# Kernel tuning notes

Hardware: AMD Instinct MI355X
Metric: run time of the kernel (lower is better)

## Reference

```python
import jax, jax.numpy as jnp
import numpy as np

B, N, D = 8, 1024, 768
H = 12
HD = D // H


def setup_inputs() -> dict:
    key = jax.random.key(0)
    ks = jax.random.split(key, 9)
    s = 1.0 / np.sqrt(D)
    return {
        "x": jax.random.normal(ks[0], (B, N, D), dtype=jnp.float32),
        "Wq": jax.random.normal(ks[1], (D, D), dtype=jnp.float32) * s,
        "bq": jax.random.normal(ks[2], (D,), dtype=jnp.float32) * 0.02,
        "Wk": jax.random.normal(ks[3], (D, D), dtype=jnp.float32) * s,
        "bk": jax.random.normal(ks[4], (D,), dtype=jnp.float32) * 0.02,
        "Wv": jax.random.normal(ks[5], (D, D), dtype=jnp.float32) * s,
        "bv": jax.random.normal(ks[6], (D,), dtype=jnp.float32) * 0.02,
        "Wo": jax.random.normal(ks[7], (D, D), dtype=jnp.float32) * s,
        "bo": jax.random.normal(ks[8], (D,), dtype=jnp.float32) * 0.02,
    }


def _softmax_one(x):
    # quiet softmax: exp(x - max) / (1 + sum exp(x - max))
    x = x - jnp.max(x, axis=-1, keepdims=True)
    ex = jnp.exp(x)
    return ex / (1.0 + jnp.sum(ex, axis=-1, keepdims=True))


def reference(x, Wq, bq, Wk, bk, Wv, bv, Wo, bo):
    q = x @ Wq + bq  # [B,N,D]
    k = x @ Wk + bk
    v = x @ Wv + bv
    # split heads -> [B,H,N,HD]
    qs = q.reshape(B, N, H, HD).transpose(0, 2, 1, 3)
    ks = k.reshape(B, N, H, HD).transpose(0, 2, 1, 3)
    vs = v.reshape(B, N, H, HD).transpose(0, 2, 1, 3)
    scores = jnp.einsum("bhqd,bhkd->bhqk", qs, ks) / np.sqrt(HD)
    attn = _softmax_one(scores)  # quiet_attention=True
    ctx = jnp.einsum("bhqk,bhkd->bhqd", attn, vs)
    ctx = ctx.transpose(0, 2, 1, 3).reshape(B, N, D)
    return ctx @ Wo + bo
```

## Files before the change

### kernel.cpp

```cpp
#include <hip/hip_runtime.h>
#include <cstdint>

#define DEV __device__ __forceinline__

typedef __bf16 bf16x4 __attribute__((ext_vector_type(4)));
typedef __bf16 bf16x8 __attribute__((ext_vector_type(8)));
typedef float  floatx4 __attribute__((ext_vector_type(4)));
typedef short  short4v __attribute__((ext_vector_type(4)));

constexpr int BB = 8, NSEQ = 1024, DMODEL = 768, NH = 12, HD = 64;
constexpr int MTOK = BB * NSEQ;
constexpr int NQKV = 3 * DMODEL;
constexpr float CS = 0.18033688011112042f;

DEV void async_copy16(void* lds, const void* g) {
    __builtin_amdgcn_global_load_lds(
        (__attribute__((address_space(1))) void*)(const_cast<void*>(g)),
        (__attribute__((address_space(3))) void*)lds,
        16, 0, 0);
}

DEV floatx4 mfma16x32(bf16x8 a, bf16x8 b, floatx4 c) {
    return __builtin_amdgcn_mfma_f32_16x16x32_bf16(a, b, c, 0, 0, 0);
}
DEV floatx4 mfma16x16(bf16x4 a, bf16x4 b, floatx4 c) {
    return __builtin_amdgcn_mfma_f32_16x16x16bf16_1k(
        __builtin_bit_cast(short4v, a), __builtin_bit_cast(short4v, b), c, 0, 0, 0);
}


__global__ __launch_bounds__(256) void k_prep(const float* __restrict__ x,
                                              __bf16* __restrict__ xb,
                                              const float* __restrict__ Wq,
                                              const float* __restrict__ Wk,
                                              const float* __restrict__ Wv,
                                              const float* __restrict__ Wo,
                                              __bf16* __restrict__ wtqkv,
                                              __bf16* __restrict__ wto,
                                              const float* __restrict__ bq,
                                              const float* __restrict__ bk,
                                              const float* __restrict__ bv,
                                              float* __restrict__ bqkv) {
    __shared__ float tile[32][33];
    int bid = blockIdx.x, t = threadIdx.x;
    if (bid < 6144) {
        int i = (bid * 256 + t) * 4;
        float4 v = *(const float4*)(x + i);
        bf16x4 o;
        o[0] = (__bf16)v.x; o[1] = (__bf16)v.y; o[2] = (__bf16)v.z; o[3] = (__bf16)v.w;
        *(bf16x4*)(xb + i) = o;
    } else if (bid < 8448) {
        int idx = bid - 6144;
        int z = idx / 576, rem = idx % 576;
        int k0 = (rem % 24) * 32, n0 = (rem / 24) * 32;
        const float* W = (z == 0) ? Wq : (z == 1) ? Wk : (z == 2) ? Wv : Wo;
        int tx = t & 31, ty = t >> 5;
#pragma unroll
        for (int p = 0; p < 4; p++)
            tile[ty + 8 * p][tx] = W[(size_t)(k0 + ty + 8 * p) * 768 + n0 + tx];
        __syncthreads();
        __bf16* out = (z < 3) ? (wtqkv + (size_t)z * 768 * 768) : wto;
#pragma unroll
        for (int p = 0; p < 4; p++)
            out[(size_t)(n0 + ty + 8 * p) * 768 + k0 + tx] = (__bf16)tile[tx][ty + 8 * p];
    } else {
        int i = (bid - 8448) * 256 + t;
        if (i < 768) bqkv[i] = bq[i];
        else if (i < 1536) bqkv[i] = bk[i - 768];
        else bqkv[i] = bv[i - 1536];
    }
}

__global__ __launch_bounds__(512) void k_qkv(const __bf16* __restrict__ A,
                                             const __bf16* __restrict__ Bt,
                                             const float* __restrict__ bias,
                                             __bf16* __restrict__ qfb,
                                             __bf16* __restrict__ kfb,
                                             __bf16* __restrict__ vfb) {
    constexpr int SLOT = 24576;
    __shared__ __align__(16) __bf16 lds[3 * SLOT];
    int t = threadIdx.x, lane = t & 63, w = t >> 6;
    int quad = lane >> 4, n16 = lane & 15;
    int wm = w >> 1, wn = w & 1;
    int m0 = blockIdx.x * 256, n0 = blockIdx.y * 128;
    floatx4 acc[4][4] = {};

    auto stage_part = [&](__bf16* slot, int k0, int p) {
        __bf16* As_ = slot;
        __bf16* Bs_ = slot + 16384;
#pragma unroll
        for (int i = 2 * p; i < 2 * p + 2; i++) {
            int off = t + i * 512;
            int row = off >> 3, pc = off & 7;
            int c = pc ^ (row & 7);
            async_copy16(&As_[row * 64 + pc * 8],
                         &A[(size_t)(m0 + row) * 768 + k0 + c * 8]);
        }
        {
            int off = t + p * 512;
            int row = off >> 3, pc = off & 7;
            int c = pc ^ (row & 7);
            async_copy16(&Bs_[row * 64 + pc * 8],
                         &Bt[(size_t)(n0 + row) * 768 + k0 + c * 8]);
        }
    };

    stage_part(lds, 0, 0);
    stage_part(lds, 0, 1);
    stage_part(lds + SLOT, 64, 0);
    stage_part(lds + SLOT, 64, 1);
    asm volatile("s_waitcnt vmcnt(6)\n\ts_barrier" ::: "memory");
    __builtin_amdgcn_sched_barrier(0);

#pragma unroll
    for (int kt = 0; kt < 12; kt++) {
        __bf16* As_ = lds + (kt % 3) * SLOT;
        __bf16* Bs_ = As_ + 16384;
        __bf16* pf = lds + ((kt + 2) % 3) * SLOT;
        int pk0 = (kt + 2) * 64;
        bool do_pf = (kt + 2 < 12);

#pragma unroll
        for (int kfi = 0; kfi < 2; kfi++) {
            if (do_pf) stage_part(pf, pk0, kfi);
            bf16x8 a[4], bfr[4];
#pragma unroll
            for (int rt = 0; rt < 4; rt++) {
                int row = wm * 64 + rt * 16 + n16;
                a[rt] = *(const bf16x8*)&As_[row * 64 + ((quad + 4 * kfi) ^ (row & 7)) * 8];
            }
#pragma unroll
            for (int ct = 0; ct < 4; ct++) {
                int row = wn * 64 + ct * 16 + n16;
                bfr[ct] = *(const bf16x8*)&Bs_[row * 64 + ((quad + 4 * kfi) ^ (row & 7)) * 8];
            }
            __builtin_amdgcn_s_setprio(1);
#pragma unroll
            for (int rt = 0; rt < 4; rt++)
#pragma unroll
                for (int ct = 0; ct < 4; ct++)
                    acc[rt][ct] = mfma16x32(a[rt], bfr[ct], acc[rt][ct]);
            __builtin_amdgcn_s_setprio(0);
        }

        if (kt < 11) {
            __builtin_amdgcn_sched_barrier(0);
            if (kt < 10) {
                asm volatile("s_waitcnt vmcnt(6)\n\ts_barrier" ::: "memory");
            } else {
                asm volatile("s_waitcnt vmcnt(0)\n\ts_barrier" ::: "memory");
            }
            __builtin_amdgcn_sched_barrier(0);
        }
    }

    if (n0 >= 1536) {
#pragma unroll
        for (int ct = 0; ct < 4; ct++) {
            int col = n0 + wn * 64 + ct * 16 + n16;
            float bs = bias[col];
            int cz = col - 1536;
            int hh = cz >> 6, hd = cz & 63;
            int mg = hd >> 4, l16 = hd & 15;
#pragma unroll
            for (int rt = 0; rt < 4; rt++) {
                int row0 = m0 + wm * 64 + rt * 16 + quad * 4;
                int bb = row0 >> 10, key = row0 & 1023;
                int ktv = key >> 6, wv = (key >> 4) & 3, qd = (key >> 2) & 3;
                bf16x4 pk;
#pragma unroll
                for (int r = 0; r < 4; r++) pk[r] = (__bf16)(acc[rt][ct][r] + bs);
                size_t idx = ((((size_t)(bb * 12 + hh) * 16 + ktv) * 4 + wv) * 4 + mg) * 256
                             + (size_t)(qd * 16 + l16) * 4;
                *(bf16x4*)&vfb[idx] = pk;
            }
        }
    } else {
        __bf16* dst = (n0 < 768) ? qfb : kfb;
        float mult = (n0 < 768) ? CS : 1.0f;
        int cofs = (n0 < 768) ? 0 : 768;
#pragma unroll
        for (int ct = 0; ct < 4; ct++) {
            int col = n0 + wn * 64 + ct * 16 + n16;
            float bs = bias[col];
            int cz = col - cofs;
            int hh = cz >> 6, hd = cz & 63;
            int kfi = hd >> 5, qd2 = (hd >> 3) & 3, j = hd & 7;
#pragma unroll
            for (int rt = 0; rt < 4; rt++) {
                int row0 = m0 + wm * 64 + rt * 16 + quad * 4;
                int bb = row0 >> 10, q = row0 & 1023;
                int t16 = q >> 4, nn = q & 15;
                size_t idx = (((size_t)(bb * 12 + hh) * 64 + t16) * 2 + kfi) * 512
                             + (size_t)(qd2 * 16 + nn) * 8 + j;
#pragma unroll
                for (int r = 0; r < 4; r++)
                    dst[idx + (size_t)r * 8] = (__bf16)((acc[rt][ct][r] + bs) * mult);
            }
        }
    }
}

template <typename OutT, bool QKV, int BN>
__global__ __launch_bounds__(256) void k_gemm(const __bf16* __restrict__ A,
                                              const __bf16* __restrict__ Bt,
                                              const float* __restrict__ bias,
                                              OutT* __restrict__ C, int Nn,
                                              __bf16* __restrict__ qfb,
                                              __bf16* __restrict__ kfb,
                                              __bf16* __restrict__ vfb) {
    constexpr int CT = BN / 32;
    constexpr int NBI = BN / 32;
    __shared__ __align__(16) __bf16 As[128 * 64];
    __shared__ __align__(16) __bf16 Bs[BN * 64];
    int t = threadIdx.x, lane = t & 63, w = t >> 6;
    int quad = lane >> 4, n16 = lane & 15;
    int wm = w & 1, wn = w >> 1;
    int m0 = blockIdx.x * 128, n0 = blockIdx.y * BN;
    floatx4 acc[4][CT] = {};

    for (int k0 = 0; k0 < 768; k0 += 64) {
        __syncthreads();
#pragma unroll
        for (int i = 0; i < 4; i++) {
            int off = t + i * 256;
            int row = off >> 3, pc = off & 7;
            int c = pc ^ (row & 7);
            async_copy16(&As[row * 64 + pc * 8],
                         &A[(size_t)(m0 + row) * 768 + k0 + c * 8]);
        }
#pragma unroll
        for (int i = 0; i < NBI; i++) {
            int off = t + i * 256;
            int row = off >> 3, pc = off & 7;
            int c = pc ^ (row & 7);
            async_copy16(&Bs[row * 64 + pc * 8],
                         &Bt[(size_t)(n0 + row) * 768 + k0 + c * 8]);
        }
        __builtin_amdgcn_s_waitcnt(0);
        __syncthreads();
#pragma unroll
        for (int kfi = 0; kfi < 2; kfi++) {
            bf16x8 a[4], bfr[CT];
#pragma unroll
            for (int rt = 0; rt < 4; rt++) {
                int row = wm * 64 + rt * 16 + n16;
                a[rt] = *(const bf16x8*)&As[row * 64 + ((quad + 4 * kfi) ^ (row & 7)) * 8];
            }
#pragma unroll
            for (int ct = 0; ct < CT; ct++) {
                int row = wn * (BN / 2) + ct * 16 + n16;
                bfr[ct] = *(const bf16x8*)&Bs[row * 64 + ((quad + 4 * kfi) ^ (row & 7)) * 8];
            }
#pragma unroll
            for (int rt = 0; rt < 4; rt++)
#pragma unroll
                for (int ct = 0; ct < CT; ct++)
                    acc[rt][ct] = mfma16x32(a[rt], bfr[ct], acc[rt][ct]);
        }
    }

    if (QKV) {
    } else {
#pragma unroll
        for (int ct = 0; ct < CT; ct++) {
            int col = n0 + wn * (BN / 2) + ct * 16 + n16;
            float bs = bias[col];
#pragma unroll
            for (int rt = 0; rt < 4; rt++) {
#pragma unroll
                for (int r = 0; r < 4; r++) {
                    int row = m0 + wm * 64 + rt * 16 + quad * 4 + r;
                    C[(size_t)row * Nn + col] = (OutT)(acc[rt][ct][r] + bs);
                }
            }
        }
    }
}

__global__ __launch_bounds__(256) void k_attn(const __bf16* __restrict__ QF,
                                              const __bf16* __restrict__ KF,
                                              const __bf16* __restrict__ VF,
                                              __bf16* __restrict__ ctx) {
    __shared__ __align__(16) unsigned char smem[18432];
    float* buf0 = (float*)smem;
    float* buf1 = (float*)(smem + 8704);
    float* Lsum = (float*)(smem + 17408);
    float* Pmax = (float*)(smem + 17920);

    int t = threadIdx.x, lane = t & 63, w = t >> 6;
    int quad = lane >> 4, n16 = lane & 15;
    int id = blockIdx.x;
    int bB = id & 7;
    int seq = id >> 3;
    int h = seq % 12;
    int qt = seq / 12;
    int q0 = qt * 32;
    int bh = bB * NH + h;

    bf16x8 qf[2][2];
    {
        const __bf16* qp = QF + (size_t)(bh * 64 + qt * 2) * 1024 + lane * 8;
#pragma unroll
        for (int ng = 0; ng < 2; ng++)
#pragma unroll
            for (int kfi = 0; kfi < 2; kfi++)
                qf[ng][kfi] = *(const bf16x8*)(qp + (ng * 2 + kfi) * 512);
    }
    const __bf16* kp = KF + (size_t)(bh * 64 + w) * 1024 + lane * 8;
    const __bf16* vp = VF + ((size_t)bh * 16 * 4 + w) * 1024 + lane * 4;

    floatx4 acc[4][2] = {};
    float rs[2] = {0.f, 0.f};
    float pm[2] = {0.f, 0.f};

    auto compute = [&](bf16x8 (&kf)[2], bf16x4 (&vf)[4]) {
        floatx4 s[2] = {};
#pragma unroll
        for (int ng = 0; ng < 2; ng++)
#pragma unroll
            for (int kfi = 0; kfi < 2; kfi++)
                s[ng] = mfma16x32(kf[kfi], qf[ng][kfi], s[ng]);
        bf16x4 pb[2];
#pragma unroll
        for (int ng = 0; ng < 2; ng++) {
#pragma unroll
            for (int r = 0; r < 4; r++) {
                float p = __builtin_amdgcn_exp2f(s[ng][r]);
                rs[ng] += p;
                pm[ng] = fmaxf(pm[ng], p);
                pb[ng][r] = (__bf16)p;
            }
        }
#pragma unroll
        for (int mg = 0; mg < 4; mg++)
#pragma unroll
            for (int ng = 0; ng < 2; ng++)
                acc[mg][ng] = mfma16x16(vf[mg], pb[ng], acc[mg][ng]);
    };

    bf16x8 kf0[2], kf1[2];
    bf16x4 vf0[4], vf1[4];
    kf0[0] = *(const bf16x8*)kp;
    kf0[1] = *(const bf16x8*)(kp + 512);
#pragma unroll
    for (int mg = 0; mg < 4; mg++) vf0[mg] = *(const bf16x4*)(vp + mg * 256);
    kp += 4096; vp += 4096;

    for (int kt = 0; kt < 16; kt += 2) {
        kf1[0] = *(const bf16x8*)kp;
        kf1[1] = *(const bf16x8*)(kp + 512);
#pragma unroll
        for (int mg = 0; mg < 4; mg++) vf1[mg] = *(const bf16x4*)(vp + mg * 256);
        kp += 4096; vp += 4096;
        compute(kf0, vf0);
        if (kt < 14) {
            kf0[0] = *(const bf16x8*)kp;
            kf0[1] = *(const bf16x8*)(kp + 512);
#pragma unroll
            for (int mg = 0; mg < 4; mg++) vf0[mg] = *(const bf16x4*)(vp + mg * 256);
            kp += 4096; vp += 4096;
        }
        compute(kf1, vf1);
    }

#pragma unroll
    for (int ng = 0; ng < 2; ng++) {
        rs[ng] += __shfl_xor(rs[ng], 16);
        rs[ng] += __shfl_xor(rs[ng], 32);
        pm[ng] = fmaxf(pm[ng], __shfl_xor(pm[ng], 16));
        pm[ng] = fmaxf(pm[ng], __shfl_xor(pm[ng], 32));
    }
    if (quad < 2) {
        Lsum[w * 32 + quad * 16 + n16] = quad ? rs[1] : rs[0];
        Pmax[w * 32 + quad * 16 + n16] = quad ? pm[1] : pm[0];
    }
    __syncthreads();

    float* mybuf = (w & 1) ? buf1 : buf0;
    if (w < 2) {
#pragma unroll
        for (int mg = 0; mg < 4; mg++)
#pragma unroll
            for (int ng = 0; ng < 2; ng++)
                *(floatx4*)&mybuf[(ng * 16 + n16) * 68 + mg * 16 + quad * 4] = acc[mg][ng];
    }
    __syncthreads();
    if (w >= 2) {
#pragma unroll
        for (int mg = 0; mg < 4; mg++)
#pragma unroll
            for (int ng = 0; ng < 2; ng++) {
                float* p = &mybuf[(ng * 16 + n16) * 68 + mg * 16 + quad * 4];
                floatx4 cur = *(const floatx4*)p;
                *(floatx4*)p = cur + acc[mg][ng];
            }
    }
    __syncthreads();

    int qrow = t >> 3;
    int hh = (t & 7) * 8;
    float l = Lsum[qrow] + Lsum[32 + qrow] + Lsum[64 + qrow] + Lsum[96 + qrow];
    float pmx = fmaxf(fmaxf(Pmax[qrow], Pmax[32 + qrow]),
                      fmaxf(Pmax[64 + qrow], Pmax[96 + qrow]));
    float invd = 1.f / (pmx + l);
    floatx4 v0 = *(const floatx4*)&buf0[qrow * 68 + hh];
    floatx4 v1 = *(const floatx4*)&buf0[qrow * 68 + hh + 4];
    floatx4 u0 = *(const floatx4*)&buf1[qrow * 68 + hh];
    floatx4 u1 = *(const floatx4*)&buf1[qrow * 68 + hh + 4];
    bf16x8 o;
#pragma unroll
    for (int j = 0; j < 4; j++) o[j] = (__bf16)((v0[j] + u0[j]) * invd);
#pragma unroll
    for (int j = 0; j < 4; j++) o[j + 4] = (__bf16)((v1[j] + u1[j]) * invd);
    __bf16* dst = ctx + (size_t)(bB * NSEQ + q0 + qrow) * DMODEL + h * 64 + hh;
    *(bf16x8*)dst = o;
}

extern "C" void kernel_launch(void* const* d_in, const int* in_sizes, int n_in,
                              void* d_out, int out_size, void* d_ws, size_t ws_size,
                              hipStream_t stream) {
    (void)in_sizes; (void)n_in; (void)out_size;
    const float* x  = (const float*)d_in[0];
    const float* Wq = (const float*)d_in[1];
    const float* bq = (const float*)d_in[2];
    const float* Wk = (const float*)d_in[3];
    const float* bk = (const float*)d_in[4];
    const float* Wv = (const float*)d_in[5];
    const float* bv = (const float*)d_in[6];
    const float* Wo = (const float*)d_in[7];
    const float* bo = (const float*)d_in[8];
    float* out = (float*)d_out;

    char* ws = (char*)d_ws;
    size_t off = 0;
    auto alloc = [&](size_t bytes) {
        void* p = ws + off;
        off += (bytes + 255) & ~(size_t)255;
        return p;
    };
    __bf16* xb    = (__bf16*)alloc((size_t)MTOK * DMODEL * 2);
    __bf16* wtqkv = (__bf16*)alloc((size_t)NQKV * DMODEL * 2);
    __bf16* wto   = (__bf16*)alloc((size_t)DMODEL * DMODEL * 2);
    float*  bqkv  = (float*)alloc((size_t)NQKV * 4);
    __bf16* qfb   = (__bf16*)alloc((size_t)MTOK * DMODEL * 2);
    __bf16* kfb   = (__bf16*)alloc((size_t)MTOK * DMODEL * 2);
    __bf16* vfb   = (__bf16*)alloc((size_t)MTOK * DMODEL * 2);
    if (off > ws_size) return;
    __bf16* ctx = xb;

    k_prep<<<dim3(8457), dim3(256), 0, stream>>>(x, xb, Wq, Wk, Wv, Wo, wtqkv, wto,
                                                 bq, bk, bv, bqkv);
    k_qkv<<<dim3(32, 18), dim3(512), 0, stream>>>(xb, wtqkv, bqkv, qfb, kfb, vfb);
    k_attn<<<dim3(3072), dim3(256), 0, stream>>>(qfb, kfb, vfb, ctx);
    k_gemm<float, false, 64><<<dim3(64, 12), dim3(256), 0, stream>>>(
        ctx, wto, bo, out, DMODEL, nullptr, nullptr, nullptr);
}
```

Measured before the change: 205.9 us.

## Switch attention to 32x32x16 MFMA with register-resident P via permlane swap

Rewrites the attention inner loop to use 32x32x16 bf16 MFMA instead of 16x16 tiles. The softmax probabilities are packed with v_cvt_pk_bf16_f32 and rearranged with v_permlane32_swap so P can feed the PV MFMA directly from registers. The Q/K/V store layouts in the QKV GEMM epilogue are changed to match the new fragment shapes. The aim is fewer MFMA issues and fewer per-element operations in the loop. It drops the sync before writing Lsum/Pmax, which relies on a later barrier for correctness.

```diff
diff --git a/kernel.cpp b/kernel.cpp
--- a/kernel.cpp
+++ b/kernel.cpp
@@ -6,7 +6,8 @@
 typedef __bf16 bf16x4 __attribute__((ext_vector_type(4)));
 typedef __bf16 bf16x8 __attribute__((ext_vector_type(8)));
 typedef float  floatx4 __attribute__((ext_vector_type(4)));
-typedef short  short4v __attribute__((ext_vector_type(4)));
+typedef float  floatx16 __attribute__((ext_vector_type(16)));
+typedef unsigned uint4v __attribute__((ext_vector_type(4)));
 
 constexpr int BB = 8, NSEQ = 1024, DMODEL = 768, NH = 12, HD = 64;
 constexpr int MTOK = BB * NSEQ;
@@ -23,9 +24,16 @@
 DEV floatx4 mfma16x32(bf16x8 a, bf16x8 b, floatx4 c) {
     return __builtin_amdgcn_mfma_f32_16x16x32_bf16(a, b, c, 0, 0, 0);
 }
-DEV floatx4 mfma16x16(bf16x4 a, bf16x4 b, floatx4 c) {
-    return __builtin_amdgcn_mfma_f32_16x16x16bf16_1k(
-        __builtin_bit_cast(short4v, a), __builtin_bit_cast(short4v, b), c, 0, 0, 0);
+DEV floatx16 mfma32x16(bf16x8 a, bf16x8 b, floatx16 c) {
+    return __builtin_amdgcn_mfma_f32_32x32x16_bf16(a, b, c, 0, 0, 0);
+}
+DEV unsigned cvtpk(float a, float b) {
+    unsigned r;
+    asm("v_cvt_pk_bf16_f32 %0, %1, %2" : "=v"(r) : "v"(a), "v"(b));
+    return r;
+}
+DEV void swap32(unsigned& x, unsigned& y) {
+    asm("v_permlane32_swap_b32 %0, %1" : "+v"(x), "+v"(y));
 }
 
 
@@ -161,38 +169,47 @@
             float bs = bias[col];
             int cz = col - 1536;
             int hh = cz >> 6, hd = cz & 63;
-            int mg = hd >> 4, l16 = hd & 15;
+            int mg = hd >> 5, l5v = hd & 31;
 #pragma unroll
             for (int rt = 0; rt < 4; rt++) {
                 int row0 = m0 + wm * 64 + rt * 16 + quad * 4;
                 int bb = row0 >> 10, key = row0 & 1023;
-                int ktv = key >> 6, wv = (key >> 4) & 3, qd = (key >> 2) & 3;
+                int iw = key >> 7, w_ = (key >> 5) & 3, kc = (key >> 4) & 1;
+                int b5v = (key >> 3) & 1, j0 = key & 7;
                 bf16x4 pk;
 #pragma unroll
                 for (int r = 0; r < 4; r++) pk[r] = (__bf16)(acc[rt][ct][r] + bs);
-                size_t idx = ((((size_t)(bb * 12 + hh) * 16 + ktv) * 4 + wv) * 4 + mg) * 256
-                             + (size_t)(qd * 16 + l16) * 4;
+                size_t idx = (((((size_t)(bb * 12 + hh) * 8 + iw) * 4 + w_) * 2 + kc) * 2 + mg) * 512
+                             + (size_t)(b5v * 32 + l5v) * 8 + j0;
                 *(bf16x4*)&vfb[idx] = pk;
             }
         }
     } else {
         __bf16* dst = (n0 < 768) ? qfb : kfb;
         float mult = (n0 < 768) ? CS : 1.0f;
-        int cofs = (n0 < 768) ? 0 : 768;
+        bool isQ = (n0 < 768);
+        int cofs = isQ ? 0 : 768;
 #pragma unroll
         for (int ct = 0; ct < 4; ct++) {
             int col = n0 + wn * 64 + ct * 16 + n16;
             float bs = bias[col];
             int cz = col - cofs;
             int hh = cz >> 6, hd = cz & 63;
-            int kfi = hd >> 5, qd2 = (hd >> 3) & 3, j = hd & 7;
+            int kfi = hd >> 4, b5v = (hd >> 3) & 1, j = hd & 7;
 #pragma unroll
             for (int rt = 0; rt < 4; rt++) {
                 int row0 = m0 + wm * 64 + rt * 16 + quad * 4;
-                int bb = row0 >> 10, q = row0 & 1023;
-                int t16 = q >> 4, nn = q & 15;
-                size_t idx = (((size_t)(bb * 12 + hh) * 64 + t16) * 2 + kfi) * 512
-                             + (size_t)(qd2 * 16 + nn) * 8 + j;
+                int bb = row0 >> 10, q10 = row0 & 1023;
+                size_t idx;
+                if (isQ) {
+                    int qt = q10 >> 5, l5v = q10 & 31;
+                    idx = (((size_t)(bb * 12 + hh) * 32 + qt) * 4 + kfi) * 512
+                          + (size_t)(b5v * 32 + l5v) * 8 + j;
+                } else {
+                    int iw = q10 >> 7, w_ = (q10 >> 5) & 3, l5v = q10 & 31;
+                    idx = ((((size_t)(bb * 12 + hh) * 8 + iw) * 4 + w_) * 4 + kfi) * 512
+                          + (size_t)(b5v * 32 + l5v) * 8 + j;
+                }
 #pragma unroll
                 for (int r = 0; r < 4; r++)
                     dst[idx + (size_t)r * 8] = (__bf16)((acc[rt][ct][r] + bs) * mult);
@@ -201,14 +218,11 @@
     }
 }
 
-template <typename OutT, bool QKV, int BN>
+template <typename OutT, int BN>
 __global__ __launch_bounds__(256) void k_gemm(const __bf16* __restrict__ A,
                                               const __bf16* __restrict__ Bt,
                                               const float* __restrict__ bias,
-                                              OutT* __restrict__ C, int Nn,
-                                              __bf16* __restrict__ qfb,
-                                              __bf16* __restrict__ kfb,
-                                              __bf16* __restrict__ vfb) {
+                                              OutT* __restrict__ C, int Nn) {
     constexpr int CT = BN / 32;
     constexpr int NBI = BN / 32;
     __shared__ __align__(16) __bf16 As[128 * 64];
@@ -260,19 +274,16 @@
         }
     }
 
-    if (QKV) {
-    } else {
-#pragma unroll
-        for (int ct = 0; ct < CT; ct++) {
-            int col = n0 + wn * (BN / 2) + ct * 16 + n16;
-            float bs = bias[col];
-#pragma unroll
-            for (int rt = 0; rt < 4; rt++) {
-#pragma unroll
-                for (int r = 0; r < 4; r++) {
-                    int row = m0 + wm * 64 + rt * 16 + quad * 4 + r;
-                    C[(size_t)row * Nn + col] = (OutT)(acc[rt][ct][r] + bs);
-                }
+#pragma unroll
+    for (int ct = 0; ct < CT; ct++) {
+        int col = n0 + wn * (BN / 2) + ct * 16 + n16;
+        float bs = bias[col];
+#pragma unroll
+        for (int rt = 0; rt < 4; rt++) {
+#pragma unroll
+            for (int r = 0; r < 4; r++) {
+                int row = m0 + wm * 64 + rt * 16 + quad * 4 + r;
+                C[(size_t)row * Nn + col] = (OutT)(acc[rt][ct][r] + bs);
             }
         }
     }
@@ -289,7 +300,7 @@
     float* Pmax = (float*)(smem + 17920);
 
     int t = threadIdx.x, lane = t & 63, w = t >> 6;
-    int quad = lane >> 4, n16 = lane & 15;
+    int l5 = lane & 31, b5 = lane >> 5;
     int id = blockIdx.x;
     int bB = id & 7;
     int seq = id >> 3;
@@ -298,102 +309,99 @@
     int q0 = qt * 32;
     int bh = bB * NH + h;
 
-    bf16x8 qf[2][2];
+    bf16x8 qf[4];
     {
-        const __bf16* qp = QF + (size_t)(bh * 64 + qt * 2) * 1024 + lane * 8;
-#pragma unroll
-        for (int ng = 0; ng < 2; ng++)
-#pragma unroll
-            for (int kfi = 0; kfi < 2; kfi++)
-                qf[ng][kfi] = *(const bf16x8*)(qp + (ng * 2 + kfi) * 512);
-    }
-    const __bf16* kp = KF + (size_t)(bh * 64 + w) * 1024 + lane * 8;
-    const __bf16* vp = VF + ((size_t)bh * 16 * 4 + w) * 1024 + lane * 4;
-
-    floatx4 acc[4][2] = {};
-    float rs[2] = {0.f, 0.f};
-    float pm[2] = {0.f, 0.f};
-
-    auto compute = [&](bf16x8 (&kf)[2], bf16x4 (&vf)[4]) {
-        floatx4 s[2] = {};
-#pragma unroll
-        for (int ng = 0; ng < 2; ng++)
-#pragma unroll
-            for (int kfi = 0; kfi < 2; kfi++)
-                s[ng] = mfma16x32(kf[kfi], qf[ng][kfi], s[ng]);
-        bf16x4 pb[2];
-#pragma unroll
-        for (int ng = 0; ng < 2; ng++) {
-#pragma unroll
-            for (int r = 0; r < 4; r++) {
-                float p = __builtin_amdgcn_exp2f(s[ng][r]);
-                rs[ng] += p;
-                pm[ng] = fmaxf(pm[ng], p);
-                pb[ng][r] = (__bf16)p;
-            }
-        }
-#pragma unroll
-        for (int mg = 0; mg < 4; mg++)
-#pragma unroll
-            for (int ng = 0; ng < 2; ng++)
-                acc[mg][ng] = mfma16x16(vf[mg], pb[ng], acc[mg][ng]);
+        const __bf16* qp = QF + ((size_t)(bh * 32 + qt) * 4) * 512 + lane * 8;
+#pragma unroll
+        for (int kfi = 0; kfi < 4; kfi++)
+            qf[kfi] = *(const bf16x8*)(qp + kfi * 512);
+    }
+    const __bf16* kp = KF + ((size_t)(bh * 8) * 4 + w) * 2048 + lane * 8;
+    const __bf16* vp = VF + ((size_t)(bh * 8) * 4 + w) * 2048 + lane * 8;
+
+    floatx16 acc[2] = {};
+    float rs = 0.f, pm = 0.f;
+
+    auto compute = [&](bf16x8 (&kf)[4], bf16x8 (&vf)[4]) {
+        floatx16 s = {};
+#pragma unroll
+        for (int kfi = 0; kfi < 4; kfi++)
+            s = mfma32x16(kf[kfi], qf[kfi], s);
+        float p[16];
+#pragma unroll
+        for (int r = 0; r < 16; r++) {
+            p[r] = __builtin_amdgcn_exp2f(s[r]);
+            rs += p[r];
+            pm = fmaxf(pm, p[r]);
+        }
+        unsigned x0 = cvtpk(p[0], p[1]),   y0 = cvtpk(p[4], p[5]);
+        unsigned x1 = cvtpk(p[2], p[3]),   y1 = cvtpk(p[6], p[7]);
+        unsigned x2 = cvtpk(p[8], p[9]),   y2 = cvtpk(p[12], p[13]);
+        unsigned x3 = cvtpk(p[10], p[11]), y3 = cvtpk(p[14], p[15]);
+        swap32(x0, y0); swap32(x1, y1); swap32(x2, y2); swap32(x3, y3);
+        uint4v pa = {x0, x1, y0, y1};
+        uint4v pbv = {x2, x3, y2, y3};
+        bf16x8 P0 = __builtin_bit_cast(bf16x8, pa);
+        bf16x8 P1 = __builtin_bit_cast(bf16x8, pbv);
+        acc[0] = mfma32x16(vf[0], P0, acc[0]);
+        acc[1] = mfma32x16(vf[1], P0, acc[1]);
+        acc[0] = mfma32x16(vf[2], P1, acc[0]);
+        acc[1] = mfma32x16(vf[3], P1, acc[1]);
     };
 
-    bf16x8 kf0[2], kf1[2];
-    bf16x4 vf0[4], vf1[4];
-    kf0[0] = *(const bf16x8*)kp;
-    kf0[1] = *(const bf16x8*)(kp + 512);
-#pragma unroll
-    for (int mg = 0; mg < 4; mg++) vf0[mg] = *(const bf16x4*)(vp + mg * 256);
-    kp += 4096; vp += 4096;
-
-    for (int kt = 0; kt < 16; kt += 2) {
-        kf1[0] = *(const bf16x8*)kp;
-        kf1[1] = *(const bf16x8*)(kp + 512);
-#pragma unroll
-        for (int mg = 0; mg < 4; mg++) vf1[mg] = *(const bf16x4*)(vp + mg * 256);
-        kp += 4096; vp += 4096;
-        compute(kf0, vf0);
-        if (kt < 14) {
-            kf0[0] = *(const bf16x8*)kp;
-            kf0[1] = *(const bf16x8*)(kp + 512);
-#pragma unroll
-            for (int mg = 0; mg < 4; mg++) vf0[mg] = *(const bf16x4*)(vp + mg * 256);
-            kp += 4096; vp += 4096;
-        }
-        compute(kf1, vf1);
-    }
-
-#pragma unroll
-    for (int ng = 0; ng < 2; ng++) {
-        rs[ng] += __shfl_xor(rs[ng], 16);
-        rs[ng] += __shfl_xor(rs[ng], 32);
-        pm[ng] = fmaxf(pm[ng], __shfl_xor(pm[ng], 16));
-        pm[ng] = fmaxf(pm[ng], __shfl_xor(pm[ng], 32));
-    }
-    if (quad < 2) {
-        Lsum[w * 32 + quad * 16 + n16] = quad ? rs[1] : rs[0];
-        Pmax[w * 32 + quad * 16 + n16] = quad ? pm[1] : pm[0];
-    }
-    __syncthreads();
+    bf16x8 ka[4], kb[4], vv[4];
+#pragma unroll
+    for (int f = 0; f < 4; f++) ka[f] = *(const bf16x8*)(kp + f * 512);
+    kp += 8192;
+
+    for (int i = 0; i < 8; i += 2) {
+#pragma unroll
+        for (int f = 0; f < 4; f++) kb[f] = *(const bf16x8*)(kp + f * 512);
+        kp += 8192;
+#pragma unroll
+        for (int f = 0; f < 4; f++) vv[f] = *(const bf16x8*)(vp + f * 512);
+        vp += 8192;
+        compute(ka, vv);
+        if (i < 6) {
+#pragma unroll
+            for (int f = 0; f < 4; f++) ka[f] = *(const bf16x8*)(kp + f * 512);
+            kp += 8192;
+        }
+#pragma unroll
+        for (int f = 0; f < 4; f++) vv[f] = *(const bf16x8*)(vp + f * 512);
+        vp += 8192;
+        compute(kb, vv);
+    }
+
+    rs += __shfl_xor(rs, 32);
+    pm = fmaxf(pm, __shfl_xor(pm, 32));
+    if (lane < 32) {
+        Lsum[w * 32 + lane] = rs;
+        Pmax[w * 32 + lane] = pm;
+    }
 
     float* mybuf = (w & 1) ? buf1 : buf0;
     if (w < 2) {
 #pragma unroll
-        for (int mg = 0; mg < 4; mg++)
-#pragma unroll
-            for (int ng = 0; ng < 2; ng++)
-                *(floatx4*)&mybuf[(ng * 16 + n16) * 68 + mg * 16 + quad * 4] = acc[mg][ng];
+        for (int mg = 0; mg < 2; mg++)
+#pragma unroll
+            for (int rq = 0; rq < 4; rq++) {
+                floatx4 v = {acc[mg][rq * 4 + 0], acc[mg][rq * 4 + 1],
+                             acc[mg][rq * 4 + 2], acc[mg][rq * 4 + 3]};
+                *(floatx4*)&mybuf[l5 * 68 + mg * 32 + b5 * 4 + rq * 8] = v;
+            }
     }
     __syncthreads();
     if (w >= 2) {
 #pragma unroll
-        for (int mg = 0; mg < 4; mg++)
-#pragma unroll
-            for (int ng = 0; ng < 2; ng++) {
-                float* p = &mybuf[(ng * 16 + n16) * 68 + mg * 16 + quad * 4];
+        for (int mg = 0; mg < 2; mg++)
+#pragma unroll
+            for (int rq = 0; rq < 4; rq++) {
+                float* p = &mybuf[l5 * 68 + mg * 32 + b5 * 4 + rq * 8];
                 floatx4 cur = *(const floatx4*)p;
-                *(floatx4*)p = cur + acc[mg][ng];
+                floatx4 v = {acc[mg][rq * 4 + 0], acc[mg][rq * 4 + 1],
+                             acc[mg][rq * 4 + 2], acc[mg][rq * 4 + 3]};
+                *(floatx4*)p = cur + v;
             }
     }
     __syncthreads();
@@ -453,6 +461,6 @@
                                                  bq, bk, bv, bqkv);
     k_qkv<<<dim3(32, 18), dim3(512), 0, stream>>>(xb, wtqkv, bqkv, qfb, kfb, vfb);
     k_attn<<<dim3(3072), dim3(256), 0, stream>>>(qfb, kfb, vfb, ctx);
-    k_gemm<float, false, 64><<<dim3(64, 12), dim3(256), 0, stream>>>(
-        ctx, wto, bo, out, DMODEL, nullptr, nullptr, nullptr);
-}
+    k_gemm<float, 64><<<dim3(64, 12), dim3(256), 0, stream>>>(
+        ctx, wto, bo, out, DMODEL);
+}
```

Measured after the change: 182.5 us. -11.4%, faster.
